# Kernel tuning notes

Measured on AMD Instinct MI355X. Metric: run time of the kernel, lower is better.

The kernel has to match this reference:

```python
import jax, jax.numpy as jnp
import numpy as np

B, L, C, H, K, P, NB = 32, 512, 512, 512, 16, 96, 4  # enc_in == hidden_size required by MlpBlockTimesteps
EPS = 1e-5


def setup_inputs() -> dict:
    key = jax.random.key(0)
    ks = jax.random.split(key, 12)
    g = lambda i, shape, s=0.02: jax.random.normal(ks[i], shape, jnp.float32) * s
    return {
        'x': jax.random.normal(ks[0], (B, L, C), jnp.float32),
        'rev_w': jnp.ones((C,), jnp.float32), 'rev_b': jnp.zeros((C,), jnp.float32),
        'mlp_w1': g(1, (L, H)), 'mlp_b1': jnp.zeros((H,), jnp.float32),
        'mlp_w2': g(2, (H, H)), 'mlp_b2': jnp.zeros((H,), jnp.float32),
        'cluster_embeds': jax.random.normal(ks[3], (K, H), jnp.float32),
        'wq': g(4, (H, H)), 'bq': jnp.zeros((H,), jnp.float32),
        'wk': g(5, (H, H)), 'bk': jnp.zeros((H,), jnp.float32),
        'wv': g(6, (H, H)), 'bv': jnp.zeros((H,), jnp.float32),
        'ts_ln_g': jnp.ones((C,), jnp.float32), 'ts_ln_b': jnp.zeros((C,), jnp.float32),
        'ts_w': g(7, (C, C)), 'ts_b': jnp.zeros((C,), jnp.float32),
        'ch_ln_g': jnp.ones((C,), jnp.float32), 'ch_ln_b': jnp.zeros((C,), jnp.float32),
        'ch_w1': g(8, (C, H)), 'ch_b1': jnp.zeros((H,), jnp.float32),
        'ch_w2': g(9, (H, C)), 'ch_b2': jnp.zeros((C,), jnp.float32),
        'out_w': g(10, (C, H, P)), 'out_b': jnp.zeros((C, P), jnp.float32),
    }


def _ln(z, g, b):
    m = z.mean(-1, keepdims=True)
    v = jnp.mean((z - m) ** 2, axis=-1, keepdims=True)
    return (z - m) / jnp.sqrt(v + EPS) * g + b


def _gelu(z):
    return jax.nn.gelu(z, approximate=False)


def _forward(x, rev_w, rev_b, mlp_w1, mlp_b1, mlp_w2, mlp_b2, cluster_embeds,
             wq, bq, wk, bk, wv, bv, ts_ln_g, ts_ln_b, ts_w, ts_b,
             ch_ln_g, ch_ln_b, ch_w1, ch_b1, ch_w2, ch_b2, out_w, out_b):
    # RevIN norm (stats over time dim=1)
    mean = x.mean(axis=1, keepdims=True)                      # [B,1,C]
    std = jnp.sqrt(jnp.var(x, axis=1, keepdims=True) + EPS)
    xn = (x - mean) / std * rev_w + rev_b                      # [B,L,C]
    xt = xn.transpose(0, 2, 1)                                 # [B,C,L]
    # channel MLP: Linear(L->H) -> ReLU -> Linear(H->H)
    h = jnp.maximum(xt @ mlp_w1 + mlp_b1, 0.0) @ mlp_w2 + mlp_b2  # [B,C,H]
    # cosine-sim soft routing + bernoulli hard mask
    cn = cluster_embeds / jnp.maximum(jnp.linalg.norm(cluster_embeds, axis=-1, keepdims=True), 1e-12)
    hn = h / jnp.maximum(jnp.linalg.norm(h, axis=-1, keepdims=True), 1e-12)
    p = jax.nn.softmax(hn @ cn.T, axis=-1)                     # [B,C,K]
    M = jax.random.bernoulli(jax.random.key(42), p).astype(h.dtype)
    # masked exp-attention over clusters
    Q = cluster_embeds @ wq + bq                               # [K,H]
    Kk = h @ wk + bk                                           # [B,C,H]
    V = h @ wv + bv
    scores = jnp.einsum('kh,bch->bkc', Q, Kk) / jnp.sqrt(jnp.float32(H))
    am = jnp.exp(scores) * M.transpose(0, 2, 1)                # [B,K,C]
    aw = am / am.sum(-1, keepdims=True)
    Cc = jnp.einsum('bkc,bch->bkh', aw, V)                     # [B,K,H]
    ce_new = jax.lax.stop_gradient(Cc.mean(0))                 # mimics .data.copy_ (no grad into C)
    # mixer block, NB iterations with shared weights (enc_in == hidden_size)
    Hm = h
    for _ in range(NB):
        z = Hm.transpose(0, 2, 1)                              # [B,H,C]
        Hm = (z + _gelu(_ln(z, ts_ln_g, ts_ln_b) @ ts_w + ts_b)).transpose(0, 2, 1)
        z = Hm.transpose(0, 2, 1)                              # [B,H,C]
        y2 = _gelu(_ln(z, ch_ln_g, ch_ln_b) @ ch_w1 + ch_b1) @ ch_w2 + ch_b2
        Hm = (z + y2).transpose(0, 2, 1)                       # [B,C,H]
    # per-channel expert projections gated by theta (uses UPDATED cluster embeds)
    theta = jnp.einsum('bck,kh->bch', p, ce_new)               # [B,C,H]
    y = jnp.einsum('bch,chp->bcp', Hm * theta, out_w) + out_b  # [B,C,P]
    y = y.transpose(0, 2, 1)                                   # [B,P,C]
    # RevIN denorm
    y = (y - rev_b) / (rev_w + EPS * EPS)
    return y * std + mean


def reference(x, rev_w, rev_b, mlp_w1, mlp_b1, mlp_w2, mlp_b2, cluster_embeds,
              wq, bq, wk, bk, wv, bv, ts_ln_g, ts_ln_b, ts_w, ts_b,
              ch_ln_g, ch_ln_b, ch_w1, ch_b1, ch_w2, ch_b2, out_w, out_b):
    return _forward(x, rev_w, rev_b, mlp_w1, mlp_b1, mlp_w2, mlp_b2, cluster_embeds,
                    wq, bq, wk, bk, wv, bv, ts_ln_g, ts_ln_b, ts_w, ts_b,
                    ch_ln_g, ch_ln_b, ch_w1, ch_b1, ch_w2, ch_b2, out_w, out_b)
```

## Files before the change

### kernel.cpp

```cpp
#include <hip/hip_runtime.h>
#include <math.h>

#define B_  32
#define L_  512
#define C_  512
#define H_  512
#define K_  16
#define P_  96
#define NB_ 4

typedef unsigned short u16;
typedef __attribute__((ext_vector_type(8))) __bf16 bf16x8;
typedef __attribute__((ext_vector_type(4))) float f32x4;


__device__ __forceinline__ float gelu_f(float x) {
    return 0.5f * x * (1.0f + erff(x * 0.70710678118654752440f));
}

__device__ __forceinline__ u16 f2bf(float f) {
    union { float f; unsigned u; } v; v.f = f;
    unsigned r = v.u + 0x7fffu + ((v.u >> 16) & 1u);
    return (u16)(r >> 16);
}
__device__ __forceinline__ float bf2f(u16 h) {
    union { unsigned u; float f; } v; v.u = ((unsigned)h) << 16;
    return v.f;
}

__device__ __forceinline__ void block_sum2_256(float& a, float& b) {
    __shared__ float la[4], lb[4];
    #pragma unroll
    for (int off = 32; off; off >>= 1) {
        a += __shfl_down(a, off);
        b += __shfl_down(b, off);
    }
    int wid = threadIdx.x >> 6;
    if ((threadIdx.x & 63) == 0) { la[wid] = a; lb[wid] = b; }
    __syncthreads();
    a = la[0] + la[1] + la[2] + la[3];
    b = lb[0] + lb[1] + lb[2] + lb[3];
}

__device__ __forceinline__ void threefry2x32(unsigned k0, unsigned k1,
                                             unsigned& x0, unsigned& x1) {
    const unsigned ks0 = k0, ks1 = k1, ks2 = k0 ^ k1 ^ 0x1BD11BDAu;
    x0 += ks0; x1 += ks1;
#define TF_ROT(v, r) (((v) << (r)) | ((v) >> (32 - (r))))
#define TF_R(r) { x0 += x1; x1 = TF_ROT(x1, r); x1 ^= x0; }
    TF_R(13) TF_R(15) TF_R(26) TF_R(6)   x0 += ks1; x1 += ks2 + 1u;
    TF_R(17) TF_R(29) TF_R(16) TF_R(24)  x0 += ks2; x1 += ks0 + 2u;
    TF_R(13) TF_R(15) TF_R(26) TF_R(6)   x0 += ks0; x1 += ks1 + 3u;
    TF_R(17) TF_R(29) TF_R(16) TF_R(24)  x0 += ks1; x1 += ks2 + 4u;
    TF_R(13) TF_R(15) TF_R(26) TF_R(6)   x0 += ks2; x1 += ks0 + 5u;
#undef TF_R
#undef TF_ROT
}

#define GLL16(g, l) __builtin_amdgcn_global_load_lds( \
    (const __attribute__((address_space(1))) void*)(g), \
    (__attribute__((address_space(3))) void*)(l), 16, 0, 0)


__global__ __launch_bounds__(256) void revin_stats(const float* __restrict__ x,
                                                   float* __restrict__ meanB,
                                                   float* __restrict__ stdB) {
    int b = blockIdx.x;
    int c = blockIdx.y * 256 + threadIdx.x;
    const float* xp = x + (size_t)b * L_ * C_ + c;
    float s = 0.f, ss = 0.f;
    for (int l = 0; l < L_; ++l) {
        float v = xp[(size_t)l * C_];
        s += v; ss += v * v;
    }
    float m = s * (1.0f / L_);
    float var = ss * (1.0f / L_) - m * m;
    meanB[b * C_ + c] = m;
    stdB[b * C_ + c]  = sqrtf(var + 1e-5f);
}

__global__ __launch_bounds__(256) void transpose_revin(const float* __restrict__ x,
                                                       const float* __restrict__ meanB,
                                                       const float* __restrict__ stdB,
                                                       const float* __restrict__ rw,
                                                       const float* __restrict__ rb,
                                                       u16* __restrict__ xt) {
    __shared__ float tile[32][33];
    int b = blockIdx.x, l0 = blockIdx.y * 32, c0 = blockIdx.z * 32;
    int tx = threadIdx.x, ty = threadIdx.y;
    for (int i = ty; i < 32; i += 8) {
        int l = l0 + i, c = c0 + tx;
        float v = x[((size_t)b * L_ + l) * C_ + c];
        v = (v - meanB[b * C_ + c]) / stdB[b * C_ + c] * rw[c] + rb[c];
        tile[i][tx] = v;
    }
    __syncthreads();
    for (int i = ty; i < 32; i += 8) {
        int c = c0 + i, l = l0 + tx;
        xt[((size_t)b * C_ + c) * L_ + l] = f2bf(tile[tx][i]);
    }
}

__global__ __launch_bounds__(256) void transpose_b(const float* __restrict__ in,
                                                   float* __restrict__ out) {
    __shared__ float tile[32][33];
    int b = blockIdx.x, r0 = blockIdx.y * 32, c0 = blockIdx.z * 32;
    int tx = threadIdx.x, ty = threadIdx.y;
    for (int i = ty; i < 32; i += 8)
        tile[i][tx] = in[((size_t)b * 512 + r0 + i) * 512 + c0 + tx];
    __syncthreads();
    for (int i = ty; i < 32; i += 8)
        out[((size_t)b * 512 + c0 + i) * 512 + r0 + tx] = tile[tx][i];
}

struct WPtrs { const float* src[7]; u16* dst[7]; };
__global__ __launch_bounds__(256) void convert_w(WPtrs wp) {
    __shared__ float tile[32][33];
    int wi = blockIdx.z;
    const float* src = wp.src[wi];
    u16* dst = wp.dst[wi];
    int r0 = blockIdx.y * 32, c0 = blockIdx.x * 32;
    int tx = threadIdx.x, ty = threadIdx.y;
    for (int i = ty; i < 32; i += 8)
        tile[i][tx] = src[(size_t)(r0 + i) * 512 + c0 + tx];
    __syncthreads();
    for (int i = ty; i < 32; i += 8)
        dst[(size_t)(c0 + i) * 512 + r0 + tx] = f2bf(tile[tx][i]);
}

template <int EPI>
__global__ __launch_bounds__(256) void gemm_bf16(const u16* __restrict__ A,
                                                 const u16* __restrict__ Bt,
                                                 const float* __restrict__ bias,
                                                 float* __restrict__ C32,
                                                 u16* __restrict__ C16,
                                                 int M, int N, int K) {
    __shared__ u16 As[128 * 32];
    __shared__ u16 Bs[128 * 32];
    int tid = threadIdx.x;
    int m0 = blockIdx.y * 128, n0 = blockIdx.x * 128;
    int lane = tid & 63, wave = tid >> 6;
    int wm = wave >> 1, wn = wave & 1;
    int col = lane & 15, quad = lane >> 4;
    int koff = quad * 8;

    int qa0 = tid, qa1 = tid + 256;
    const u16* Ag0 = A + (size_t)(m0 + (qa0 >> 2)) * K + (qa0 & 3) * 8;
    const u16* Ag1 = A + (size_t)(m0 + (qa1 >> 2)) * K + (qa1 & 3) * 8;
    const u16* Bg0 = Bt + (size_t)(n0 + (qa0 >> 2)) * K + (qa0 & 3) * 8;
    const u16* Bg1 = Bt + (size_t)(n0 + (qa1 >> 2)) * K + (qa1 & 3) * 8;
    u16* Al0 = &As[qa0 * 8];
    u16* Al1 = &As[qa1 * 8];
    u16* Bl0 = &Bs[qa0 * 8];
    u16* Bl1 = &Bs[qa1 * 8];

    f32x4 acc[4][4];
    #pragma unroll
    for (int i = 0; i < 4; ++i)
        #pragma unroll
        for (int j = 0; j < 4; ++j)
            acc[i][j] = (f32x4){0.f, 0.f, 0.f, 0.f};

    for (int k0 = 0; k0 < K; k0 += 32) {
        GLL16(Ag0 + k0, Al0);
        GLL16(Ag1 + k0, Al1);
        GLL16(Bg0 + k0, Bl0);
        GLL16(Bg1 + k0, Bl1);
        __syncthreads();
        bf16x8 af[4], bfr[4];
        #pragma unroll
        for (int mt = 0; mt < 4; ++mt)
            af[mt] = *(const bf16x8*)&As[(wm * 64 + mt * 16 + col) * 32 + koff];
        #pragma unroll
        for (int nt = 0; nt < 4; ++nt)
            bfr[nt] = *(const bf16x8*)&Bs[(wn * 64 + nt * 16 + col) * 32 + koff];
        #pragma unroll
        for (int mt = 0; mt < 4; ++mt)
            #pragma unroll
            for (int nt = 0; nt < 4; ++nt)
                acc[mt][nt] = __builtin_amdgcn_mfma_f32_16x16x32_bf16(
                    af[mt], bfr[nt], acc[mt][nt], 0, 0, 0);
        __syncthreads();
    }

    float bb[4];
    #pragma unroll
    for (int nt = 0; nt < 4; ++nt) bb[nt] = bias[n0 + wn * 64 + nt * 16 + col];
    #pragma unroll
    for (int mt = 0; mt < 4; ++mt) {
        int mbase = m0 + wm * 64 + mt * 16 + quad * 4;
        #pragma unroll
        for (int r = 0; r < 4; ++r) {
            size_t rowoff = (size_t)(mbase + r) * N;
            #pragma unroll
            for (int nt = 0; nt < 4; ++nt) {
                int gn = n0 + wn * 64 + nt * 16 + col;
                float t = acc[mt][nt][r] + bb[nt];
                if (EPI == 1) t = fmaxf(t, 0.f);
                if (EPI == 2 || EPI == 3) t = gelu_f(t);
                if (EPI == 0) {
                    C32[rowoff + gn] = t;
                } else if (EPI == 1 || EPI == 2 || EPI == 6) {
                    C16[rowoff + gn] = f2bf(t);
                } else if (EPI == 3 || EPI == 4) {
                    C32[rowoff + gn] += t;
                } else if (EPI == 5) {
                    C32[rowoff + gn] = t;
                    C16[rowoff + gn] = f2bf(t);
                }
            }
        }
    }
}

__global__ __launch_bounds__(256) void gemm_f32(const float* __restrict__ A,
                                                const float* __restrict__ Bm,
                                                const float* __restrict__ bias,
                                                float* __restrict__ Cm,
                                                int M, int N, int K) {
    __shared__ float As[16][64];
    __shared__ float Bs[16][64];
    int tid = threadIdx.x;
    int tx = tid & 15, ty = tid >> 4;
    int m0 = blockIdx.y * 64, n0 = blockIdx.x * 64;
    float acc[4][4] = {};
    for (int k0 = 0; k0 < K; k0 += 16) {
        {
            int r = tid >> 2, cc = (tid & 3) * 4, gm = m0 + r;
            float4 v = make_float4(0.f, 0.f, 0.f, 0.f);
            if (gm < M) v = *(const float4*)(A + (size_t)gm * K + k0 + cc);
            As[cc + 0][r] = v.x; As[cc + 1][r] = v.y;
            As[cc + 2][r] = v.z; As[cc + 3][r] = v.w;
        }
        {
            int r = tid >> 4, cc = (tid & 15) * 4;
            *(float4*)&Bs[r][cc] = *(const float4*)(Bm + (size_t)(k0 + r) * N + n0 + cc);
        }
        __syncthreads();
        #pragma unroll
        for (int kk = 0; kk < 16; ++kk) {
            float4 a4 = *(const float4*)&As[kk][ty * 4];
            float4 b4 = *(const float4*)&Bs[kk][tx * 4];
            float av[4] = {a4.x, a4.y, a4.z, a4.w};
            float bv[4] = {b4.x, b4.y, b4.z, b4.w};
            #pragma unroll
            for (int i = 0; i < 4; ++i)
                #pragma unroll
                for (int j = 0; j < 4; ++j)
                    acc[i][j] += av[i] * bv[j];
        }
        __syncthreads();
    }
    int gn = n0 + tx * 4;
    float4 b4 = *(const float4*)(bias + gn);
    float bb[4] = {b4.x, b4.y, b4.z, b4.w};
    #pragma unroll
    for (int i = 0; i < 4; ++i) {
        int gm = m0 + ty * 4 + i;
        if (gm >= M) break;
        float* cp = Cm + (size_t)gm * N + gn;
        *(float4*)cp = make_float4(acc[i][0] + bb[0], acc[i][1] + bb[1],
                                   acc[i][2] + bb[2], acc[i][3] + bb[3]);
    }
}

__global__ __launch_bounds__(256) void ln_rows(const float* __restrict__ in,
                                               u16* __restrict__ out,
                                               const float* __restrict__ g,
                                               const float* __restrict__ b) {
    int row = blockIdx.x, tid = threadIdx.x;
    float2 v = ((const float2*)(in + (size_t)row * 512))[tid];
    float s = v.x + v.y, ss = v.x * v.x + v.y * v.y;
    block_sum2_256(s, ss);
    float mean = s * (1.0f / 512.0f);
    float var  = ss * (1.0f / 512.0f) - mean * mean;
    float rstd = rsqrtf(var + 1e-5f);
    float2 gv = ((const float2*)g)[tid];
    float2 bv = ((const float2*)b)[tid];
    ushort2 o;
    o.x = f2bf((v.x - mean) * rstd * gv.x + bv.x);
    o.y = f2bf((v.y - mean) * rstd * gv.y + bv.y);
    ((ushort2*)(out + (size_t)row * 512))[tid] = o;
}

__global__ __launch_bounds__(256) void normalize_rows16(const float* __restrict__ ce,
                                                        float* __restrict__ cn) {
    int k = blockIdx.x, tid = threadIdx.x;
    float2 v = ((const float2*)(ce + (size_t)k * 512))[tid];
    float ss = v.x * v.x + v.y * v.y, dummy = 0.f;
    block_sum2_256(ss, dummy);
    float inv = 1.0f / fmaxf(sqrtf(ss), 1e-12f);
    float2 o; o.x = v.x * inv; o.y = v.y * inv;
    ((float2*)(cn + (size_t)k * 512))[tid] = o;
}

__global__ __launch_bounds__(256) void routing_kernel(const float* __restrict__ h,
                                                      const float* __restrict__ cn,
                                                      float* __restrict__ p) {
    int tid = threadIdx.x;
    int r = tid >> 4, k = tid & 15;
    int row = blockIdx.x * 16 + r;
    const float4* hp = (const float4*)(h + (size_t)row * 512);
    const float4* ck = (const float4*)(cn + (size_t)k * 512);
    float ss = 0.f;
    #pragma unroll
    for (int j = k * 8; j < k * 8 + 8; ++j) {
        float4 v = hp[j];
        ss += v.x * v.x + v.y * v.y + v.z * v.z + v.w * v.w;
    }
    #pragma unroll
    for (int off = 8; off; off >>= 1) ss += __shfl_xor(ss, off, 16);
    float inv = 1.0f / fmaxf(sqrtf(ss), 1e-12f);
    float d = 0.f;
    for (int j = 0; j < 128; ++j) {
        float4 a = hp[j], b = ck[j];
        d += a.x * b.x + a.y * b.y + a.z * b.z + a.w * b.w;
    }
    d *= inv;
    float mx = d;
    #pragma unroll
    for (int off = 8; off; off >>= 1) mx = fmaxf(mx, __shfl_xor(mx, off, 16));
    float e = expf(d - mx);
    float s = e;
    #pragma unroll
    for (int off = 8; off; off >>= 1) s += __shfl_xor(s, off, 16);
    p[(size_t)row * 16 + k] = e / s;
}

__global__ __launch_bounds__(256) void attn_scores(const float* __restrict__ Kk,
                                                   const float* __restrict__ Q,
                                                   const float* __restrict__ pbuf,
                                                   float* __restrict__ am) {
    int tid = threadIdx.x;
    int k = tid >> 4, r = tid & 15;
    int row = blockIdx.x * 16 + r;
    int b = row >> 9, c = row & 511;
    const float4* kp = (const float4*)(Kk + (size_t)row * 512);
    const float4* qp = (const float4*)(Q + (size_t)k * 512);
    float d = 0.f;
    for (int j = 0; j < 128; ++j) {
        float4 a = kp[j], q = qp[j];
        d += a.x * q.x + a.y * q.y + a.z * q.z + a.w * q.w;
    }
    d *= 0.044194173824159216f;
    int j = row * 16 + k;
    const int HALF = (B_ * C_ * K_) / 2;
    unsigned x0 = (j < HALF) ? (unsigned)j : (unsigned)(j - HALF);
    unsigned x1 = x0 + (unsigned)HALF;
    threefry2x32(0u, 42u, x0, x1);
    unsigned bits = (j < HALF) ? x0 : x1;
    float u = __uint_as_float((bits >> 9) | 0x3f800000u) - 1.0f;
    float m = (u < pbuf[j]) ? 1.0f : 0.0f;
    am[((size_t)b * 16 + k) * 512 + c] = expf(d) * m;
}

__global__ __launch_bounds__(256) void row_recip(const float* __restrict__ am,
                                                 float* __restrict__ recip) {
    int rk = blockIdx.x, tid = threadIdx.x;
    float2 v = ((const float2*)(am + (size_t)rk * 512))[tid];
    float s = v.x + v.y, dummy = 0.f;
    block_sum2_256(s, dummy);
    if (tid == 0) recip[rk] = 1.0f / s;
}

__global__ __launch_bounds__(256) void cc_partial(const float* __restrict__ am,
                                                  const float* __restrict__ recip,
                                                  const u16* __restrict__ V16,
                                                  float* __restrict__ Ccp) {
    int b = blockIdx.x, cs = blockIdx.y;
    int c0 = cs * 64, tid = threadIdx.x;
    __shared__ float awS[16 * 64];
    for (int idx = tid; idx < 1024; idx += 256) {
        int k = idx >> 6, cj = idx & 63;
        awS[idx] = am[((size_t)b * 16 + k) * 512 + c0 + cj] * recip[b * 16 + k];
    }
    __syncthreads();
    float acc0[16] = {}, acc1[16] = {};
    for (int cj = 0; cj < 64; ++cj) {
        const u16* vp = V16 + ((size_t)(b * 512) + c0 + cj) * 512;
        unsigned pk = ((const unsigned*)vp)[tid];
        float v0 = bf2f((u16)(pk & 0xffffu));
        float v1 = bf2f((u16)(pk >> 16));
        #pragma unroll
        for (int k = 0; k < 16; ++k) {
            float a = awS[k * 64 + cj];
            acc0[k] += a * v0;
            acc1[k] += a * v1;
        }
    }
    float* out = Ccp + ((size_t)(b * 8 + cs)) * 8192;
    #pragma unroll
    for (int k = 0; k < 16; ++k) {
        float2 o; o.x = acc0[k]; o.y = acc1[k];
        ((float2*)(out + k * 512))[tid] = o;
    }
}

__global__ __launch_bounds__(256) void cc_mean(const float* __restrict__ Ccp,
                                               float* __restrict__ ce) {
    int idx = blockIdx.x * 256 + threadIdx.x;
    float s = 0.f;
    for (int sl = 0; sl < 256; ++sl) s += Ccp[(size_t)sl * 8192 + idx];
    ce[idx] = s * (1.0f / B_);
}

__global__ __launch_bounds__(256) void out_partial(const float* __restrict__ Hm,
                                                   const float* __restrict__ pbuf,
                                                   const float* __restrict__ ce,
                                                   const float* __restrict__ out_w,
                                                   float* __restrict__ Pp) {
    int c = blockIdx.x, hs = blockIdx.y, tid = threadIdx.x;
    int h0 = hs * 128;
    __shared__ float wS[32 * 96];
    __shared__ float gS[32 * 33];
    __shared__ float ceS[16 * 32];
    __shared__ float pS[32 * 16];
    for (int idx = tid; idx < 512; idx += 256) {
        int b = idx >> 4, k = idx & 15;
        pS[idx] = pbuf[((size_t)(b * 512 + c)) * 16 + k];
    }
    int b_own = tid >> 3, pb = (tid & 7) * 12;
    float acc[12] = {};
    const size_t wbase = (size_t)c * 512 * 96;
    for (int hc = 0; hc < 4; ++hc) {
        int hh0 = h0 + hc * 32;
        __syncthreads();
        for (int idx = tid; idx < 768; idx += 256)
            ((float4*)wS)[idx] = ((const float4*)(out_w + wbase + (size_t)hh0 * 96))[idx];
        for (int idx = tid; idx < 512; idx += 256) {
            int k = idx >> 5, hh = idx & 31;
            ceS[idx] = ce[k * 512 + hh0 + hh];
        }
        __syncthreads();
        {
            int b = tid >> 3, hq = (tid & 7) * 4;
            float4 hv = *(const float4*)(Hm + ((size_t)(b * 512 + c)) * 512 + hh0 + hq);
            float hvv[4] = {hv.x, hv.y, hv.z, hv.w};
            #pragma unroll
            for (int j = 0; j < 4; ++j) {
                float s = 0.f;
                #pragma unroll
                for (int k = 0; k < 16; ++k) s += pS[b * 16 + k] * ceS[k * 32 + hq + j];
                gS[b * 33 + hq + j] = hvv[j] * s;
            }
        }
        __syncthreads();
        #pragma unroll 8
        for (int hh = 0; hh < 32; ++hh) {
            float g = gS[b_own * 33 + hh];
            #pragma unroll
            for (int j = 0; j < 12; ++j) acc[j] += g * wS[hh * 96 + pb + j];
        }
    }
    float* pp = Pp + ((size_t)hs * 512 + c) * 3072 + b_own * 96 + pb;
    #pragma unroll
    for (int j = 0; j < 12; ++j) pp[j] = acc[j];
}

__global__ __launch_bounds__(256) void out_final(const float* __restrict__ Pp,
                                                 const float* __restrict__ out_b,
                                                 const float* __restrict__ rev_w,
                                                 const float* __restrict__ rev_b,
                                                 const float* __restrict__ meanB,
                                                 const float* __restrict__ stdB,
                                                 float* __restrict__ out) {
    int c = blockIdx.x, tid = threadIdx.x;
    float inv_rw = 1.0f / (rev_w[c] + 1e-10f);
    float rb = rev_b[c];
    for (int idx = tid; idx < 3072; idx += 256) {
        int b = idx / 96, p = idx - b * 96;
        float v = out_b[(size_t)c * 96 + p];
        #pragma unroll
        for (int hs = 0; hs < 4; ++hs)
            v += Pp[((size_t)hs * 512 + c) * 3072 + idx];
        float y = (v - rb) * inv_rw * stdB[b * 512 + c] + meanB[b * 512 + c];
        out[((size_t)b * 96 + p) * 512 + c] = y;
    }
}


extern "C" void kernel_launch(void* const* d_in, const int* in_sizes, int n_in,
                              void* d_out, int out_size, void* d_ws, size_t ws_size,
                              hipStream_t stream) {
    const float* x        = (const float*)d_in[0];
    const float* rev_w    = (const float*)d_in[1];
    const float* rev_b    = (const float*)d_in[2];
    const float* mlp_w1   = (const float*)d_in[3];
    const float* mlp_b1   = (const float*)d_in[4];
    const float* mlp_w2   = (const float*)d_in[5];
    const float* mlp_b2   = (const float*)d_in[6];
    const float* clu_emb  = (const float*)d_in[7];
    const float* wq       = (const float*)d_in[8];
    const float* bq       = (const float*)d_in[9];
    const float* wk       = (const float*)d_in[10];
    const float* bk       = (const float*)d_in[11];
    const float* wv       = (const float*)d_in[12];
    const float* bv       = (const float*)d_in[13];
    const float* ts_ln_g  = (const float*)d_in[14];
    const float* ts_ln_b  = (const float*)d_in[15];
    const float* ts_w     = (const float*)d_in[16];
    const float* ts_b     = (const float*)d_in[17];
    const float* ch_ln_g  = (const float*)d_in[18];
    const float* ch_ln_b  = (const float*)d_in[19];
    const float* ch_w1    = (const float*)d_in[20];
    const float* ch_b1    = (const float*)d_in[21];
    const float* ch_w2    = (const float*)d_in[22];
    const float* ch_b2    = (const float*)d_in[23];
    const float* out_w    = (const float*)d_in[24];
    const float* out_b    = (const float*)d_in[25];

    float* f = (float*)d_ws;
    const size_t SLOT = (size_t)(B_ * C_) * H_;
    float* F0 = f;
    float* F1 = f + SLOT;
    u16*  X16 = (u16*)(f + 2 * SLOT);
    u16*  T16 = (u16*)(f + 2 * SLOT + SLOT / 2);
    float* sm = f + 3 * SLOT;
    u16* Wt[7];
    for (int i = 0; i < 7; ++i) { Wt[i] = (u16*)sm; sm += 131072; }
    float* meanB  = sm; sm += B_ * C_;
    float* stdB   = sm; sm += B_ * C_;
    float* pbuf   = sm; sm += B_ * C_ * K_;
    float* ambuf  = sm; sm += B_ * K_ * C_;
    float* recips = sm; sm += B_ * K_;
    float* cebuf  = sm; sm += K_ * H_;
    float* cnbuf  = sm; sm += K_ * H_;
    float* Qbuf   = sm; sm += K_ * H_;
    float* Ccp = F1;
    float* Pp  = F1;

    dim3 ggrid(4, 128);
    dim3 t_grid(B_, 16, 16);
    dim3 t_blk(32, 8);
    const int Mrows = B_ * C_;

    revin_stats<<<dim3(B_, 2), 256, 0, stream>>>(x, meanB, stdB);
    transpose_revin<<<t_grid, t_blk, 0, stream>>>(x, meanB, stdB, rev_w, rev_b, X16);
    WPtrs wp;
    wp.src[0] = mlp_w1; wp.src[1] = mlp_w2; wp.src[2] = wk; wp.src[3] = wv;
    wp.src[4] = ts_w;   wp.src[5] = ch_w1;  wp.src[6] = ch_w2;
    for (int i = 0; i < 7; ++i) wp.dst[i] = Wt[i];
    convert_w<<<dim3(16, 16, 7), t_blk, 0, stream>>>(wp);
    gemm_f32<<<dim3(8, 1), 256, 0, stream>>>(clu_emb, wq, bq, Qbuf, K_, H_, H_);
    gemm_bf16<1><<<ggrid, 256, 0, stream>>>(X16, Wt[0], mlp_b1, nullptr, T16,
                                            Mrows, H_, L_);
    gemm_bf16<5><<<ggrid, 256, 0, stream>>>(T16, Wt[1], mlp_b2, F0, X16,
                                            Mrows, H_, H_);
    normalize_rows16<<<K_, 256, 0, stream>>>(clu_emb, cnbuf);
    routing_kernel<<<Mrows / 16, 256, 0, stream>>>(F0, cnbuf, pbuf);
    gemm_bf16<0><<<ggrid, 256, 0, stream>>>(X16, Wt[2], bk, F1, nullptr,
                                            Mrows, H_, H_);
    gemm_bf16<6><<<ggrid, 256, 0, stream>>>(X16, Wt[3], bv, nullptr, T16,
                                            Mrows, H_, H_);
    attn_scores<<<Mrows / 16, 256, 0, stream>>>(F1, Qbuf, pbuf, ambuf);
    row_recip<<<B_ * K_, 256, 0, stream>>>(ambuf, recips);
    cc_partial<<<dim3(B_, 8), 256, 0, stream>>>(ambuf, recips, T16, Ccp);
    cc_mean<<<(K_ * H_) / 256, 256, 0, stream>>>(Ccp, cebuf);
    transpose_b<<<t_grid, t_blk, 0, stream>>>(F0, F1);
    for (int it = 0; it < NB_; ++it) {
        ln_rows<<<Mrows, 256, 0, stream>>>(F1, T16, ts_ln_g, ts_ln_b);
        gemm_bf16<3><<<ggrid, 256, 0, stream>>>(T16, Wt[4], ts_b, F1, nullptr,
                                                Mrows, C_, C_);
        ln_rows<<<Mrows, 256, 0, stream>>>(F1, T16, ch_ln_g, ch_ln_b);
        gemm_bf16<2><<<ggrid, 256, 0, stream>>>(T16, Wt[5], ch_b1, nullptr, X16,
                                                Mrows, H_, C_);
        gemm_bf16<4><<<ggrid, 256, 0, stream>>>(X16, Wt[6], ch_b2, F1, nullptr,
                                                Mrows, C_, H_);
    }
    transpose_b<<<t_grid, t_blk, 0, stream>>>(F1, F0);
    out_partial<<<dim3(C_, 4), 256, 0, stream>>>(F0, pbuf, cebuf, out_w, Pp);
    out_final<<<C_, 256, 0, stream>>>(Pp, out_b, rev_w, rev_b, meanB, stdB,
                                      (float*)d_out);
}
```

Baseline: 1.171 ms.

## Fuse mixer blocks into one register-resident kernel and use MFMA for output projection

Replaces the 20 per-iteration launches (LayerNorm, three GEMMs with residual epilogues) with a single kernel. Each block keeps 32 rows of the activation in registers across all four mixer iterations, computes LayerNorm stats in place, and streams the bf16 weights from global memory for each GEMM. This removes repeated round trips of the fp32 activation through memory. The output projection also moves from a scalar fp32 FMA kernel plus a separate reduction kernel to one MFMA kernel that converts out_w to bf16 on the fly and applies the denorm in its epilogue. The trade-offs are only 512 blocks with high register use, weights re-read by every block with no LDS tiling, and bf16 rounding of the out_w multiply.

Result: no change. 1.170 ms (-0.1%).

```diff
diff --git a/kernel.cpp b/kernel.cpp
--- a/kernel.cpp
+++ b/kernel.cpp
@@ -197,13 +197,10 @@
                 int gn = n0 + wn * 64 + nt * 16 + col;
                 float t = acc[mt][nt][r] + bb[nt];
                 if (EPI == 1) t = fmaxf(t, 0.f);
-                if (EPI == 2 || EPI == 3) t = gelu_f(t);
                 if (EPI == 0) {
                     C32[rowoff + gn] = t;
-                } else if (EPI == 1 || EPI == 2 || EPI == 6) {
+                } else if (EPI == 1 || EPI == 6) {
                     C16[rowoff + gn] = f2bf(t);
-                } else if (EPI == 3 || EPI == 4) {
-                    C32[rowoff + gn] += t;
                 } else if (EPI == 5) {
                     C32[rowoff + gn] = t;
                     C16[rowoff + gn] = f2bf(t);
@@ -264,25 +261,6 @@
     }
 }
 
-__global__ __launch_bounds__(256) void ln_rows(const float* __restrict__ in,
-                                               u16* __restrict__ out,
-                                               const float* __restrict__ g,
-                                               const float* __restrict__ b) {
-    int row = blockIdx.x, tid = threadIdx.x;
-    float2 v = ((const float2*)(in + (size_t)row * 512))[tid];
-    float s = v.x + v.y, ss = v.x * v.x + v.y * v.y;
-    block_sum2_256(s, ss);
-    float mean = s * (1.0f / 512.0f);
-    float var  = ss * (1.0f / 512.0f) - mean * mean;
-    float rstd = rsqrtf(var + 1e-5f);
-    float2 gv = ((const float2*)g)[tid];
-    float2 bv = ((const float2*)b)[tid];
-    ushort2 o;
-    o.x = f2bf((v.x - mean) * rstd * gv.x + bv.x);
-    o.y = f2bf((v.y - mean) * rstd * gv.y + bv.y);
-    ((ushort2*)(out + (size_t)row * 512))[tid] = o;
-}
-
 __global__ __launch_bounds__(256) void normalize_rows16(const float* __restrict__ ce,
                                                         float* __restrict__ cn) {
     int k = blockIdx.x, tid = threadIdx.x;
@@ -404,75 +382,279 @@
     ce[idx] = s * (1.0f / B_);
 }
 
-__global__ __launch_bounds__(256) void out_partial(const float* __restrict__ Hm,
-                                                   const float* __restrict__ pbuf,
-                                                   const float* __restrict__ ce,
-                                                   const float* __restrict__ out_w,
-                                                   float* __restrict__ Pp) {
-    int c = blockIdx.x, hs = blockIdx.y, tid = threadIdx.x;
-    int h0 = hs * 128;
-    __shared__ float wS[32 * 96];
-    __shared__ float gS[32 * 33];
-    __shared__ float ceS[16 * 32];
+__global__ __launch_bounds__(256) void mixer_fused(
+    float* __restrict__ z,
+    const u16* __restrict__ tsw, const u16* __restrict__ chw1,
+    const u16* __restrict__ chw2,
+    const float* __restrict__ tslng, const float* __restrict__ tslnb,
+    const float* __restrict__ tsb,
+    const float* __restrict__ chlng, const float* __restrict__ chlnb,
+    const float* __restrict__ chb1, const float* __restrict__ chb2) {
+    __shared__ u16 A16[32 * 520];
+    __shared__ float statS[32 * 2];
+    __shared__ float partS[4 * 32 * 2];
+    __shared__ float vecS[7 * 512];
+
+    int tid = threadIdx.x, lane = tid & 63, wave = tid >> 6;
+    int col = lane & 15, quad = lane >> 4;
+    int m0 = blockIdx.x * 32;
+
+    {
+        const float* vsrc[7] = {tslng, tslnb, tsb, chlng, chlnb, chb1, chb2};
+        for (int i = tid; i < 7 * 512; i += 256) vecS[i] = vsrc[i >> 9][i & 511];
+    }
+
+    f32x4 zr[16];
+    float* zbase = z + (size_t)m0 * 512;
+    #pragma unroll
+    for (int mt = 0; mt < 2; ++mt)
+        #pragma unroll
+        for (int nt = 0; nt < 8; ++nt)
+            #pragma unroll
+            for (int r = 0; r < 4; ++r)
+                zr[mt * 8 + nt][r] =
+                    zbase[(size_t)(mt * 16 + quad * 4 + r) * 512 +
+                          wave * 128 + nt * 16 + col];
+
+    auto stats = [&]() {
+        #pragma unroll
+        for (int mt = 0; mt < 2; ++mt)
+            #pragma unroll
+            for (int r = 0; r < 4; ++r) {
+                float s = 0.f, ss = 0.f;
+                #pragma unroll
+                for (int nt = 0; nt < 8; ++nt) {
+                    float v = zr[mt * 8 + nt][r];
+                    s += v; ss += v * v;
+                }
+                #pragma unroll
+                for (int o = 8; o; o >>= 1) {
+                    s += __shfl_xor(s, o, 16);
+                    ss += __shfl_xor(ss, o, 16);
+                }
+                if (col == 0) {
+                    int m = mt * 16 + quad * 4 + r;
+                    partS[(wave * 32 + m) * 2 + 0] = s;
+                    partS[(wave * 32 + m) * 2 + 1] = ss;
+                }
+            }
+        __syncthreads();
+        if (tid < 32) {
+            float s = 0.f, ss = 0.f;
+            #pragma unroll
+            for (int w = 0; w < 4; ++w) {
+                s += partS[(w * 32 + tid) * 2];
+                ss += partS[(w * 32 + tid) * 2 + 1];
+            }
+            float mean = s * (1.0f / 512.0f);
+            float var = ss * (1.0f / 512.0f) - mean * mean;
+            statS[tid * 2] = mean;
+            statS[tid * 2 + 1] = rsqrtf(var + 1e-5f);
+        }
+        __syncthreads();
+    };
+
+    auto writeNorm = [&](int gi, int bi) {
+        float mn[8], rs[8];
+        #pragma unroll
+        for (int mt = 0; mt < 2; ++mt)
+            #pragma unroll
+            for (int r = 0; r < 4; ++r) {
+                int m = mt * 16 + quad * 4 + r;
+                mn[mt * 4 + r] = statS[m * 2];
+                rs[mt * 4 + r] = statS[m * 2 + 1];
+            }
+        #pragma unroll
+        for (int nt = 0; nt < 8; ++nt) {
+            int n = wave * 128 + nt * 16 + col;
+            float g = vecS[gi * 512 + n], bb = vecS[bi * 512 + n];
+            #pragma unroll
+            for (int mt = 0; mt < 2; ++mt)
+                #pragma unroll
+                for (int r = 0; r < 4; ++r) {
+                    int m = mt * 16 + quad * 4 + r;
+                    float v = (zr[mt * 8 + nt][r] - mn[mt * 4 + r]) *
+                              rs[mt * 4 + r] * g + bb;
+                    A16[m * 520 + n] = f2bf(v);
+                }
+        }
+        __syncthreads();
+    };
+
+    f32x4 acc[16];
+    auto gemm = [&](const u16* __restrict__ W) {
+        #pragma unroll
+        for (int i = 0; i < 16; ++i) acc[i] = (f32x4){0.f, 0.f, 0.f, 0.f};
+        #pragma unroll 4
+        for (int kc = 0; kc < 16; ++kc) {
+            bf16x8 a0 = *(const bf16x8*)&A16[col * 520 + kc * 32 + quad * 8];
+            bf16x8 a1 = *(const bf16x8*)&A16[(16 + col) * 520 + kc * 32 + quad * 8];
+            #pragma unroll
+            for (int nt = 0; nt < 8; ++nt) {
+                bf16x8 bf = *(const bf16x8*)
+                    &W[(size_t)(wave * 128 + nt * 16 + col) * 512 + kc * 32 + quad * 8];
+                acc[nt] = __builtin_amdgcn_mfma_f32_16x16x32_bf16(a0, bf, acc[nt], 0, 0, 0);
+                acc[8 + nt] = __builtin_amdgcn_mfma_f32_16x16x32_bf16(a1, bf, acc[8 + nt], 0, 0, 0);
+            }
+        }
+    };
+
+    for (int it = 0; it < NB_; ++it) {
+        stats();
+        writeNorm(0, 1);
+        gemm(tsw);
+        #pragma unroll
+        for (int nt = 0; nt < 8; ++nt) {
+            float bb = vecS[2 * 512 + wave * 128 + nt * 16 + col];
+            #pragma unroll
+            for (int mt = 0; mt < 2; ++mt)
+                #pragma unroll
+                for (int r = 0; r < 4; ++r)
+                    zr[mt * 8 + nt][r] += gelu_f(acc[mt * 8 + nt][r] + bb);
+        }
+        stats();
+        writeNorm(3, 4);
+        gemm(chw1);
+        __syncthreads();
+        #pragma unroll
+        for (int nt = 0; nt < 8; ++nt) {
+            int n = wave * 128 + nt * 16 + col;
+            float bb = vecS[5 * 512 + n];
+            #pragma unroll
+            for (int mt = 0; mt < 2; ++mt)
+                #pragma unroll
+                for (int r = 0; r < 4; ++r) {
+                    int m = mt * 16 + quad * 4 + r;
+                    A16[m * 520 + n] = f2bf(gelu_f(acc[mt * 8 + nt][r] + bb));
+                }
+        }
+        __syncthreads();
+        gemm(chw2);
+        #pragma unroll
+        for (int nt = 0; nt < 8; ++nt) {
+            float bb = vecS[6 * 512 + wave * 128 + nt * 16 + col];
+            #pragma unroll
+            for (int mt = 0; mt < 2; ++mt)
+                #pragma unroll
+                for (int r = 0; r < 4; ++r)
+                    zr[mt * 8 + nt][r] += acc[mt * 8 + nt][r] + bb;
+        }
+    }
+
+    #pragma unroll
+    for (int mt = 0; mt < 2; ++mt)
+        #pragma unroll
+        for (int nt = 0; nt < 8; ++nt)
+            #pragma unroll
+            for (int r = 0; r < 4; ++r)
+                zbase[(size_t)(mt * 16 + quad * 4 + r) * 512 +
+                      wave * 128 + nt * 16 + col] = zr[mt * 8 + nt][r];
+}
+
+__global__ __launch_bounds__(256) void outproj_mfma(
+    const float* __restrict__ Hm, const float* __restrict__ pbuf,
+    const float* __restrict__ ce, const float* __restrict__ out_w,
+    const float* __restrict__ out_b, const float* __restrict__ rev_w,
+    const float* __restrict__ rev_b, const float* __restrict__ meanB,
+    const float* __restrict__ stdB, float* __restrict__ out) {
     __shared__ float pS[32 * 16];
+    __shared__ u16 A16[32 * 520];
+    __shared__ u16 Bs[4][96 * 40];
+    __shared__ float redS[4][32 * 96];
+
+    int c = blockIdx.x, tid = threadIdx.x;
+    int lane = tid & 63, wave = tid >> 6;
+    int col = lane & 15, quad = lane >> 4;
+
     for (int idx = tid; idx < 512; idx += 256) {
         int b = idx >> 4, k = idx & 15;
         pS[idx] = pbuf[((size_t)(b * 512 + c)) * 16 + k];
     }
-    int b_own = tid >> 3, pb = (tid & 7) * 12;
-    float acc[12] = {};
+    __syncthreads();
+
+    {
+        int h0 = lane * 8;
+        f32x4 th[8][2];
+        #pragma unroll
+        for (int b = 0; b < 8; ++b) {
+            th[b][0] = (f32x4){0.f, 0.f, 0.f, 0.f};
+            th[b][1] = (f32x4){0.f, 0.f, 0.f, 0.f};
+        }
+        for (int k = 0; k < 16; ++k) {
+            f32x4 ce0 = *(const f32x4*)&ce[k * 512 + h0];
+            f32x4 ce1 = *(const f32x4*)&ce[k * 512 + h0 + 4];
+            #pragma unroll
+            for (int b = 0; b < 8; ++b) {
+                float pk = pS[(wave * 8 + b) * 16 + k];
+                th[b][0] += ce0 * pk;
+                th[b][1] += ce1 * pk;
+            }
+        }
+        #pragma unroll
+        for (int b = 0; b < 8; ++b) {
+            int bb = wave * 8 + b;
+            const f32x4* hp = (const f32x4*)&Hm[((size_t)(bb * 512 + c)) * 512 + h0];
+            f32x4 g0 = hp[0] * th[b][0];
+            f32x4 g1 = hp[1] * th[b][1];
+            ushort4 o0, o1;
+            o0.x = f2bf(g0[0]); o0.y = f2bf(g0[1]); o0.z = f2bf(g0[2]); o0.w = f2bf(g0[3]);
+            o1.x = f2bf(g1[0]); o1.y = f2bf(g1[1]); o1.z = f2bf(g1[2]); o1.w = f2bf(g1[3]);
+            *(ushort4*)&A16[bb * 520 + h0] = o0;
+            *(ushort4*)&A16[bb * 520 + h0 + 4] = o1;
+        }
+    }
+    __syncthreads();
+
+    f32x4 pacc[12];
+    #pragma unroll
+    for (int i = 0; i < 12; ++i) pacc[i] = (f32x4){0.f, 0.f, 0.f, 0.f};
     const size_t wbase = (size_t)c * 512 * 96;
-    for (int hc = 0; hc < 4; ++hc) {
-        int hh0 = h0 + hc * 32;
-        __syncthreads();
-        for (int idx = tid; idx < 768; idx += 256)
-            ((float4*)wS)[idx] = ((const float4*)(out_w + wbase + (size_t)hh0 * 96))[idx];
-        for (int idx = tid; idx < 512; idx += 256) {
-            int k = idx >> 5, hh = idx & 31;
-            ceS[idx] = ce[k * 512 + hh0 + hh];
-        }
-        __syncthreads();
+    for (int i = 0; i < 4; ++i) {
+        int kc = wave * 4 + i;
         {
-            int b = tid >> 3, hq = (tid & 7) * 4;
-            float4 hv = *(const float4*)(Hm + ((size_t)(b * 512 + c)) * 512 + hh0 + hq);
-            float hvv[4] = {hv.x, hv.y, hv.z, hv.w};
-            #pragma unroll
-            for (int j = 0; j < 4; ++j) {
-                float s = 0.f;
-                #pragma unroll
-                for (int k = 0; k < 16; ++k) s += pS[b * 16 + k] * ceS[k * 32 + hq + j];
-                gS[b * 33 + hq + j] = hvv[j] * s;
-            }
-        }
-        __syncthreads();
-        #pragma unroll 8
-        for (int hh = 0; hh < 32; ++hh) {
-            float g = gS[b_own * 33 + hh];
-            #pragma unroll
-            for (int j = 0; j < 12; ++j) acc[j] += g * wS[hh * 96 + pb + j];
-        }
-    }
-    float* pp = Pp + ((size_t)hs * 512 + c) * 3072 + b_own * 96 + pb;
-    #pragma unroll
-    for (int j = 0; j < 12; ++j) pp[j] = acc[j];
-}
-
-__global__ __launch_bounds__(256) void out_final(const float* __restrict__ Pp,
-                                                 const float* __restrict__ out_b,
-                                                 const float* __restrict__ rev_w,
-                                                 const float* __restrict__ rev_b,
-                                                 const float* __restrict__ meanB,
-                                                 const float* __restrict__ stdB,
-                                                 float* __restrict__ out) {
-    int c = blockIdx.x, tid = threadIdx.x;
+            const float4* wsrc = (const float4*)(out_w + wbase + (size_t)kc * 32 * 96);
+            #pragma unroll
+            for (int t = 0; t < 12; ++t) {
+                int flat4 = lane + t * 64;
+                float4 v = wsrc[flat4];
+                int kk = flat4 / 24, p4 = (flat4 % 24) * 4;
+                Bs[wave][(p4 + 0) * 40 + kk] = f2bf(v.x);
+                Bs[wave][(p4 + 1) * 40 + kk] = f2bf(v.y);
+                Bs[wave][(p4 + 2) * 40 + kk] = f2bf(v.z);
+                Bs[wave][(p4 + 3) * 40 + kk] = f2bf(v.w);
+            }
+        }
+        __syncthreads();
+        #pragma unroll
+        for (int mt = 0; mt < 2; ++mt) {
+            bf16x8 a = *(const bf16x8*)&A16[(mt * 16 + col) * 520 + kc * 32 + quad * 8];
+            #pragma unroll
+            for (int nt = 0; nt < 6; ++nt) {
+                bf16x8 bf = *(const bf16x8*)&Bs[wave][(nt * 16 + col) * 40 + quad * 8];
+                pacc[mt * 6 + nt] = __builtin_amdgcn_mfma_f32_16x16x32_bf16(
+                    a, bf, pacc[mt * 6 + nt], 0, 0, 0);
+            }
+        }
+        __syncthreads();
+    }
+    #pragma unroll
+    for (int mt = 0; mt < 2; ++mt)
+        #pragma unroll
+        for (int nt = 0; nt < 6; ++nt)
+            #pragma unroll
+            for (int r = 0; r < 4; ++r) {
+                int b = mt * 16 + quad * 4 + r;
+                int p = nt * 16 + col;
+                redS[wave][b * 96 + p] = pacc[mt * 6 + nt][r];
+            }
+    __syncthreads();
+
     float inv_rw = 1.0f / (rev_w[c] + 1e-10f);
     float rb = rev_b[c];
-    for (int idx = tid; idx < 3072; idx += 256) {
-        int b = idx / 96, p = idx - b * 96;
-        float v = out_b[(size_t)c * 96 + p];
-        #pragma unroll
-        for (int hs = 0; hs < 4; ++hs)
-            v += Pp[((size_t)hs * 512 + c) * 3072 + idx];
+    for (int e = tid; e < 3072; e += 256) {
+        float v = redS[0][e] + redS[1][e] + redS[2][e] + redS[3][e];
+        int b = e / 96, p = e - b * 96;
+        v += out_b[(size_t)c * 96 + p];
         float y = (v - rb) * inv_rw * stdB[b * 512 + c] + meanB[b * 512 + c];
         out[((size_t)b * 96 + p) * 512 + c] = y;
     }
@@ -527,7 +709,6 @@
     float* cnbuf  = sm; sm += K_ * H_;
     float* Qbuf   = sm; sm += K_ * H_;
     float* Ccp = F1;
-    float* Pp  = F1;
 
     dim3 ggrid(4, 128);
     dim3 t_grid(B_, 16, 16);
@@ -557,18 +738,11 @@
     cc_partial<<<dim3(B_, 8), 256, 0, stream>>>(ambuf, recips, T16, Ccp);
     cc_mean<<<(K_ * H_) / 256, 256, 0, stream>>>(Ccp, cebuf);
     transpose_b<<<t_grid, t_blk, 0, stream>>>(F0, F1);
-    for (int it = 0; it < NB_; ++it) {
-        ln_rows<<<Mrows, 256, 0, stream>>>(F1, T16, ts_ln_g, ts_ln_b);
-        gemm_bf16<3><<<ggrid, 256, 0, stream>>>(T16, Wt[4], ts_b, F1, nullptr,
-                                                Mrows, C_, C_);
-        ln_rows<<<Mrows, 256, 0, stream>>>(F1, T16, ch_ln_g, ch_ln_b);
-        gemm_bf16<2><<<ggrid, 256, 0, stream>>>(T16, Wt[5], ch_b1, nullptr, X16,
-                                                Mrows, H_, C_);
-        gemm_bf16<4><<<ggrid, 256, 0, stream>>>(X16, Wt[6], ch_b2, F1, nullptr,
-                                                Mrows, C_, H_);
-    }
+    mixer_fused<<<Mrows / 32, 256, 0, stream>>>(F1, Wt[4], Wt[5], Wt[6],
+                                                ts_ln_g, ts_ln_b, ts_b,
+                                                ch_ln_g, ch_ln_b, ch_b1, ch_b2);
     transpose_b<<<t_grid, t_blk, 0, stream>>>(F1, F0);
-    out_partial<<<dim3(C_, 4), 256, 0, stream>>>(F0, pbuf, cebuf, out_w, Pp);
-    out_final<<<C_, 256, 0, stream>>>(Pp, out_b, rev_w, rev_b, meanB, stdB,
-                                      (float*)d_out);
-}
+    outproj_mfma<<<C_, 256, 0, stream>>>(F0, pbuf, cebuf, out_w, out_b,
+                                         rev_w, rev_b, meanB, stdB,
+                                         (float*)d_out);
+}
```
